# Kernel optimization log

Hardware: AMD Instinct MI355X
Metric: run time of the kernel (lower is better)

## Reference

```python
import jax, jax.numpy as jnp
import numpy as np

N_NODES = 50000
N_EDGES = 600000
D_IN = 128
H = 128
D_OUT = 1


def setup_inputs() -> dict:
    key = jax.random.key(0)
    ks = jax.random.split(key, 6)
    x = jax.random.normal(ks[0], (N_NODES, D_IN), dtype=jnp.float32)
    edge_index = jax.random.randint(ks[1], (2, N_EDGES), 0, N_NODES, dtype=jnp.int32)
    # Glorot-ish init for GCN weights
    W1 = jax.random.normal(ks[2], (D_IN, H), dtype=jnp.float32) / np.sqrt(D_IN)
    W2 = jax.random.normal(ks[3], (H, H), dtype=jnp.float32) / np.sqrt(H)
    W3 = jax.random.normal(ks[4], (H, D_OUT), dtype=jnp.float32) / np.sqrt(H)
    b1 = jnp.zeros((H,), jnp.float32)
    b2 = jnp.zeros((H,), jnp.float32)
    b3 = jnp.zeros((D_OUT,), jnp.float32)
    return {"x": x, "edge_index": edge_index, "W1": W1, "b1": b1,
            "W2": W2, "b2": b2, "W3": W3, "b3": b3}


def _gcn_layer(h, src, dst, norm, self_norm, W, b, n_nodes):
    # GCNConv: h' = D^{-1/2}(A+I)D^{-1/2} (h W) + b
    hw = h @ W                                        # [N, F_out]
    msg = hw[src] * norm[:, None]                     # [E, F_out] edge gather
    agg = jax.ops.segment_sum(msg, dst, num_segments=n_nodes)
    agg = agg + hw * self_norm[:, None]               # self-loop contribution
    return agg + b


def reference(x, edge_index, W1, b1, W2, b2, W3, b3):
    # NOTE: F.dropout treated as identity (deterministic eval reference).
    n = x.shape[0]
    src, dst = edge_index[0], edge_index[1]
    # symmetric normalization with self-loops (PyG gcn_norm, edge_weight=1)
    deg = jnp.zeros((n,), x.dtype).at[dst].add(1.0) + 1.0
    dis = jax.lax.rsqrt(deg)                          # deg^{-1/2}
    norm = dis[src] * dis[dst]                        # per-edge norm
    self_norm = dis * dis
    h = jax.nn.relu(_gcn_layer(x, src, dst, norm, self_norm, W1, b1, n))
    h = jax.nn.relu(_gcn_layer(h, src, dst, norm, self_norm, W2, b2, n))
    h = jax.nn.relu(_gcn_layer(h, src, dst, norm, self_norm, W3, b3, n))
    return h
```

## Files before the change

kernel.cpp:

```cpp
#include <hip/hip_runtime.h>
#include <hip/hip_fp16.h>


typedef _Float16 v8h __attribute__((ext_vector_type(8)));
typedef float v4f __attribute__((ext_vector_type(4)));

__global__ __launch_bounds__(256) void k_zero_wcast(int* __restrict__ cnt8, int n8,
                                                    int BZ,
                                                    const float* __restrict__ W1,
                                                    const float* __restrict__ W2,
                                                    __half* __restrict__ Wt1,
                                                    __half* __restrict__ Wt2) {
    int b = blockIdx.x;
    if (b < BZ) {
        int i = b * 256 + threadIdx.x;
        if (i < n8) cnt8[i] = 0;
    } else {
        int i = (b - BZ) * 256 + threadIdx.x;
        int k = i >> 7, c = i & 127;
        Wt1[c * 128 + k] = __float2half(W1[i]);
        Wt2[c * 128 + k] = __float2half(W2[i]);
    }
}

__global__ __launch_bounds__(256) void k_count_gemm(const int* __restrict__ dst,
                                                    int* __restrict__ cnt8,
                                                    int* __restrict__ rank, int nE,
                                                    int BE, int nN,
                                                    const float* __restrict__ X32,
                                                    const __half* __restrict__ Wt,
                                                    __half* __restrict__ HWS,
                                                    int nrows) {
    __shared__ __half xs[64 * 136];
    if (blockIdx.x < BE) {
        int e = blockIdx.x * 256 + threadIdx.x;
        if (e < nE) {
            int bank = blockIdx.x & 7;
            rank[e] = atomicAdd(&cnt8[bank * nN + dst[e]], 1);
        }
        return;
    }

    const int t = threadIdx.x;
    const int row0 = (blockIdx.x - BE) * 64;

#pragma unroll
    for (int i = 0; i < 8; ++i) {
        int f = t + i * 256;
        int r = f >> 5, k4 = f & 31;
        int gr = row0 + r;
        float4 v = make_float4(0.f, 0.f, 0.f, 0.f);
        if (gr < nrows) v = ((const float4*)X32)[(size_t)gr * 32 + k4];
        __half2 h01 = __float22half2_rn(make_float2(v.x, v.y));
        __half2 h23 = __float22half2_rn(make_float2(v.z, v.w));
        float2 packed;
        *(__half2*)&packed.x = h01;
        *(__half2*)&packed.y = h23;
        *(float2*)&xs[r * 136 + k4 * 4] = packed;
    }
    __syncthreads();

    const int w = t >> 6;
    const int l = t & 63;
    const int mrow = l & 15;
    const int kq = l >> 4;

    v8h a[4];
#pragma unroll
    for (int kk = 0; kk < 4; ++kk)
        a[kk] = *(const v8h*)&xs[(w * 16 + mrow) * 136 + kk * 32 + kq * 8];

    v4f acc[8];
#pragma unroll
    for (int c = 0; c < 8; ++c) acc[c] = (v4f){0.f, 0.f, 0.f, 0.f};

#pragma unroll
    for (int kk = 0; kk < 4; ++kk) {
#pragma unroll
        for (int c = 0; c < 8; ++c) {
            v8h b = *(const v8h*)&Wt[(size_t)(c * 16 + mrow) * 128 + kk * 32 + kq * 8];
            acc[c] = __builtin_amdgcn_mfma_f32_16x16x32_f16(a[kk], b, acc[c], 0, 0, 0);
        }
    }

#pragma unroll
    for (int c = 0; c < 8; ++c) {
#pragma unroll
        for (int r = 0; r < 4; ++r) {
            int grow = row0 + w * 16 + kq * 4 + r;
            if (grow < nrows)
                HWS[(size_t)grow * 128 + c * 16 + mrow] = __float2half(acc[c][r]);
        }
    }
}

__global__ __launch_bounds__(256) void k_scan_blk(const int* __restrict__ cnt8,
                                                  float* __restrict__ dis,
                                                  int* __restrict__ excl,
                                                  int* __restrict__ blk_sum, int nN) {
    __shared__ int sm[256];
    const int t = threadIdx.x;
    int i = blockIdx.x * 256 + t;
    int v = 0;
    if (i < nN) {
#pragma unroll
        for (int b = 0; b < 8; ++b) v += cnt8[b * nN + i];
        dis[i] = rsqrtf((float)v + 1.0f);
    }
    sm[t] = v;
    __syncthreads();
#pragma unroll
    for (int off = 1; off < 256; off <<= 1) {
        int x = (t >= off) ? sm[t - off] : 0;
        __syncthreads();
        sm[t] += x;
        __syncthreads();
    }
    if (i < nN) excl[i] = sm[t] - v;
    if (t == 255) blk_sum[blockIdx.x] = sm[255];
}

__global__ __launch_bounds__(256) void k_scan_add(const int* __restrict__ excl,
                                                  const int* __restrict__ blk_sum,
                                                  const int* __restrict__ cnt8,
                                                  int* __restrict__ row_ptr,
                                                  int* __restrict__ base8,
                                                  int nN, int nB) {
    __shared__ int sm[256];
    const int t = threadIdx.x;
    int v = (t < nB) ? blk_sum[t] : 0;
    sm[t] = v;
    __syncthreads();
#pragma unroll
    for (int off = 1; off < 256; off <<= 1) {
        int x = (t >= off) ? sm[t - off] : 0;
        __syncthreads();
        sm[t] += x;
        __syncthreads();
    }
    int i = blockIdx.x * 256 + t;
    if (i < nN) {
        int b = i >> 8;
        int rp = excl[i] + sm[b] - blk_sum[b];
        row_ptr[i] = rp;
        int off = rp;
#pragma unroll
        for (int bk = 0; bk < 8; ++bk) {
            base8[i * 8 + bk] = off;
            off += cnt8[bk * nN + i];
        }
    }
    if (i == 0) row_ptr[nN] = sm[255];
}

__global__ __launch_bounds__(256) void k_bin(const int* __restrict__ src,
                                             const int* __restrict__ dst,
                                             const int* __restrict__ rank,
                                             const int* __restrict__ base8,
                                             int* __restrict__ src_csr, int nE) {
    int e = blockIdx.x * 256 + threadIdx.x;
    if (e < nE) {
        int d = dst[e];
        int bank = blockIdx.x & 7;
        src_csr[base8[d * 8 + bank] + rank[e]] = src[e];
    }
}

__device__ __forceinline__ void add8(float acc[8], float4 r) {
    __half2* hp = (__half2*)&r;
#pragma unroll
    for (int k = 0; k < 4; ++k) {
        float2 f = __half22float2(hp[k]);
        acc[2 * k] += f.x;
        acc[2 * k + 1] += f.y;
    }
}

__device__ __forceinline__ void add8w(float acc[8], float4 r, float w) {
    __half2* hp = (__half2*)&r;
#pragma unroll
    for (int k = 0; k < 4; ++k) {
        float2 f = __half22float2(hp[k]);
        acc[2 * k] = fmaf(f.x, w, acc[2 * k]);
        acc[2 * k + 1] = fmaf(f.y, w, acc[2 * k + 1]);
    }
}

__device__ __forceinline__ void gather_row16(const float4* __restrict__ Hv,
                                             const int* __restrict__ row_ptr,
                                             const int* __restrict__ src_csr,
                                             int g, int f8, float acc[8]) {
    int beg = row_ptr[g], end = row_ptr[g + 1];
#pragma unroll
    for (int k = 0; k < 8; ++k) acc[k] = 0.f;
    add8(acc, Hv[(size_t)g * 16 + f8]);
    int e = beg;
    for (; e + 4 <= end; e += 4) {
        int s[4];
#pragma unroll
        for (int j = 0; j < 4; ++j) s[j] = src_csr[e + j];
        float4 r[4];
#pragma unroll
        for (int j = 0; j < 4; ++j) r[j] = Hv[(size_t)s[j] * 16 + f8];
#pragma unroll
        for (int j = 0; j < 4; ++j) add8(acc, r[j]);
    }
    for (; e < end; ++e) add8(acc, Hv[(size_t)src_csr[e] * 16 + f8]);
}

__device__ __forceinline__ void gather_row16w(const float4* __restrict__ Hv,
                                              const int* __restrict__ row_ptr,
                                              const int* __restrict__ src_csr,
                                              const float* __restrict__ dis,
                                              int g, float dg, int f8,
                                              float acc[8]) {
    int beg = row_ptr[g], end = row_ptr[g + 1];
#pragma unroll
    for (int k = 0; k < 8; ++k) acc[k] = 0.f;
    add8w(acc, Hv[(size_t)g * 16 + f8], dg);
    int e = beg;
    for (; e + 4 <= end; e += 4) {
        int s[4];
#pragma unroll
        for (int j = 0; j < 4; ++j) s[j] = src_csr[e + j];
        float wv[4];
#pragma unroll
        for (int j = 0; j < 4; ++j) wv[j] = dis[s[j]];
        float4 r[4];
#pragma unroll
        for (int j = 0; j < 4; ++j) r[j] = Hv[(size_t)s[j] * 16 + f8];
#pragma unroll
        for (int j = 0; j < 4; ++j) add8w(acc, r[j], wv[j]);
    }
    for (; e < end; ++e) {
        int s = src_csr[e];
        add8w(acc, Hv[(size_t)s * 16 + f8], dis[s]);
    }
}

__global__ __launch_bounds__(512) void k_gather_gemm(const __half* __restrict__ HWS1,
                                                     const int* __restrict__ row_ptr,
                                                     const int* __restrict__ src_csr,
                                                     const float* __restrict__ dis,
                                                     const float* __restrict__ bias,
                                                     const __half* __restrict__ Wt,
                                                     __half* __restrict__ HWS2,
                                                     int nN) {
    __shared__ __half xs[64 * 136];
    __shared__ int q;
    const int t = threadIdx.x;
    const int row0 = blockIdx.x * 64;
    const int l = t & 63;
    const int f8 = t & 15;
    const int qbase = l & 48;
    const float4* Hv = (const float4*)HWS1;

    float bv[8];
    *(float4*)&bv[0] = ((const float4*)bias)[f8 * 2];
    *(float4*)&bv[4] = ((const float4*)bias)[f8 * 2 + 1];

    if (t == 0) q = 0;
    __syncthreads();

    for (;;) {
        int lr = 0;
        if (f8 == 0) lr = atomicAdd(&q, 1);
        lr = __shfl(lr, qbase, 64);
        if (lr >= 64) break;
        int g = row0 + lr;
        float acc[8];
        __half2 h[4];
        if (g < nN) {
            float dn = dis[g];
            gather_row16w(Hv, row_ptr, src_csr, dis, g, dn, f8, acc);
#pragma unroll
            for (int k = 0; k < 4; ++k)
                h[k] = __float22half2_rn(make_float2(
                    fmaxf(acc[2 * k] * dn + bv[2 * k], 0.f),
                    fmaxf(acc[2 * k + 1] * dn + bv[2 * k + 1], 0.f)));
        } else {
#pragma unroll
            for (int k = 0; k < 4; ++k) h[k] = __float2half2_rn(0.f);
        }
        *(float4*)&xs[lr * 136 + f8 * 8] = *(float4*)h;
    }
    __syncthreads();

    const int w = t >> 6;
    const int mrow = l & 15;
    const int kq = l >> 4;
    const int rgrp = (w & 3) * 16;
    const int cgrp = (w >> 2) * 4;

    v8h a[4];
#pragma unroll
    for (int kk = 0; kk < 4; ++kk)
        a[kk] = *(const v8h*)&xs[(rgrp + mrow) * 136 + kk * 32 + kq * 8];

    v4f acc[4];
#pragma unroll
    for (int c = 0; c < 4; ++c) acc[c] = (v4f){0.f, 0.f, 0.f, 0.f};

#pragma unroll
    for (int kk = 0; kk < 4; ++kk) {
#pragma unroll
        for (int c = 0; c < 4; ++c) {
            v8h b = *(const v8h*)&Wt[(size_t)((cgrp + c) * 16 + mrow) * 128 + kk * 32 + kq * 8];
            acc[c] = __builtin_amdgcn_mfma_f32_16x16x32_f16(a[kk], b, acc[c], 0, 0, 0);
        }
    }

    float dn4[4];
#pragma unroll
    for (int r = 0; r < 4; ++r) {
        int grow = row0 + rgrp + kq * 4 + r;
        dn4[r] = (grow < nN) ? dis[grow] : 0.f;
    }
#pragma unroll
    for (int c = 0; c < 4; ++c) {
#pragma unroll
        for (int r = 0; r < 4; ++r) {
            int grow = row0 + rgrp + kq * 4 + r;
            if (grow < nN)
                HWS2[(size_t)grow * 128 + (cgrp + c) * 16 + mrow] =
                    __float2half(acc[c][r] * dn4[r]);
        }
    }
}

__global__ __launch_bounds__(256) void k_gather_gemv(const __half* __restrict__ HWS2,
                                                     const int* __restrict__ row_ptr,
                                                     const int* __restrict__ src_csr,
                                                     const float* __restrict__ dis,
                                                     const float* __restrict__ bias,
                                                     const float* __restrict__ W3,
                                                     float* __restrict__ hw3s, int nN) {
    int g = blockIdx.x * 16 + (threadIdx.x >> 4);
    if (g >= nN) return;
    int f8 = threadIdx.x & 15;
    float acc[8];
    gather_row16((const float4*)HWS2, row_ptr, src_csr, g, f8, acc);
    float dn = dis[g];
    float bv[8], w3[8];
    *(float4*)&bv[0] = ((const float4*)bias)[f8 * 2];
    *(float4*)&bv[4] = ((const float4*)bias)[f8 * 2 + 1];
    *(float4*)&w3[0] = ((const float4*)W3)[f8 * 2];
    *(float4*)&w3[4] = ((const float4*)W3)[f8 * 2 + 1];
    float sum = 0.f;
#pragma unroll
    for (int k = 0; k < 8; ++k)
        sum += fmaxf(acc[k] * dn + bv[k], 0.f) * w3[k];
#pragma unroll
    for (int off = 8; off > 0; off >>= 1) sum += __shfl_down(sum, off, 16);
    if (f8 == 0) hw3s[g] = sum * dn;
}

__global__ __launch_bounds__(256) void k_gather3(const float* __restrict__ hw3s,
                                                 const int* __restrict__ row_ptr,
                                                 const int* __restrict__ src_csr,
                                                 const float* __restrict__ dis,
                                                 const float* __restrict__ b3,
                                                 float* __restrict__ out, int nN) {
    int i = blockIdx.x * 256 + threadIdx.x;
    if (i >= nN) return;
    float acc = hw3s[i];
    int beg = row_ptr[i], end = row_ptr[i + 1];
    for (int e = beg; e < end; ++e) acc += hw3s[src_csr[e]];
    out[i] = fmaxf(acc * dis[i] + b3[0], 0.f);
}

extern "C" void kernel_launch(void* const* d_in, const int* in_sizes, int n_in,
                              void* d_out, int out_size, void* d_ws, size_t ws_size,
                              hipStream_t stream) {
    const float* x  = (const float*)d_in[0];
    const int*   ei = (const int*)d_in[1];
    const float* W1 = (const float*)d_in[2];
    const float* b1 = (const float*)d_in[3];
    const float* W2 = (const float*)d_in[4];
    const float* b2 = (const float*)d_in[5];
    const float* W3 = (const float*)d_in[6];
    const float* b3 = (const float*)d_in[7];

    const int nN = in_sizes[0] / 128;
    const int nE = in_sizes[1] / 2;
    const int* src = ei;
    const int* dst = ei + nE;

    const int nB = (nN + 255) / 256;

    char* p = (char*)d_ws;
    int*    cnt8     = (int*)p;           p += (size_t)nN * 8 * 4;
    int*    base8    = (int*)p;           p += (size_t)nN * 8 * 4;
    int*    excl     = (int*)p;           p += (size_t)nN * 4;
    int*    blk_sum  = (int*)p;           p += (size_t)(nB + 1) * 4;
    int*    row_ptr  = (int*)p;           p += (size_t)(nN + 1) * 4;
    int*    rank     = (int*)p;           p += (size_t)nE * 4;
    int*    src_csr  = (int*)p;           p += (size_t)nE * 4;
    float*  dis      = (float*)p;         p += (size_t)nN * 4;
    float*  hw3s     = (float*)p;         p += (size_t)nN * 4;
    p = (char*)(((uintptr_t)p + 255) & ~(uintptr_t)255);
    __half* Wt1      = (__half*)p;        p += (size_t)128 * 128 * 2;
    __half* Wt2      = (__half*)p;        p += (size_t)128 * 128 * 2;
    __half* bufA     = (__half*)p;        p += (size_t)nN * 128 * 2;
    p = (char*)(((uintptr_t)p + 255) & ~(uintptr_t)255);
    __half* bufB     = (__half*)p;        p += (size_t)nN * 128 * 2;

    const int BE  = (nE + 255) / 256;
    const int BN  = (nN + 255) / 256;
    const int BG  = (nN + 63) / 64;
    const int BGV = (nN + 15) / 16;
    const int BZ8 = (nN * 8 + 255) / 256;

    k_zero_wcast<<<BZ8 + 64, 256, 0, stream>>>(cnt8, nN * 8, BZ8, W1, W2, Wt1, Wt2);

    k_count_gemm<<<BE + BG, 256, 0, stream>>>(dst, cnt8, rank, nE, BE, nN,
                                              x, Wt1, bufA, nN);

    k_scan_blk<<<nB, 256, 0, stream>>>(cnt8, dis, excl, blk_sum, nN);
    k_scan_add<<<nB, 256, 0, stream>>>(excl, blk_sum, cnt8, row_ptr, base8, nN, nB);

    k_bin<<<BE, 256, 0, stream>>>(src, dst, rank, base8, src_csr, nE);

    k_gather_gemm<<<BG, 512, 0, stream>>>(bufA, row_ptr, src_csr, dis, b1, Wt2,
                                          bufB, nN);

    k_gather_gemv<<<BGV, 256, 0, stream>>>(bufB, row_ptr, src_csr, dis, b2, W3,
                                           hw3s, nN);

    k_gather3<<<BN, 256, 0, stream>>>(hw3s, row_ptr, src_csr, dis, b3,
                                      (float*)d_out, nN);
}
```

Baseline: 222.6 us.

## Prescale layer-1 GEMM output by dis and fuse it with CSR binning

```diff
diff --git a/kernel.cpp b/kernel.cpp
--- a/kernel.cpp
+++ b/kernel.cpp
@@ -23,26 +23,100 @@
     }
 }
 
-__global__ __launch_bounds__(256) void k_count_gemm(const int* __restrict__ dst,
-                                                    int* __restrict__ cnt8,
-                                                    int* __restrict__ rank, int nE,
-                                                    int BE, int nN,
-                                                    const float* __restrict__ X32,
-                                                    const __half* __restrict__ Wt,
-                                                    __half* __restrict__ HWS,
-                                                    int nrows) {
+__global__ __launch_bounds__(256) void k_count(const int* __restrict__ dst,
+                                               int* __restrict__ cnt8,
+                                               int* __restrict__ rank,
+                                               int nE, int nN) {
+    int e = blockIdx.x * 256 + threadIdx.x;
+    if (e < nE) {
+        int bank = blockIdx.x & 7;
+        rank[e] = atomicAdd(&cnt8[bank * nN + dst[e]], 1);
+    }
+}
+
+__global__ __launch_bounds__(256) void k_scan_blk(const int* __restrict__ cnt8,
+                                                  float* __restrict__ dis,
+                                                  int* __restrict__ excl,
+                                                  int* __restrict__ blk_sum, int nN) {
+    __shared__ int sm[256];
+    const int t = threadIdx.x;
+    int i = blockIdx.x * 256 + t;
+    int v = 0;
+    if (i < nN) {
+#pragma unroll
+        for (int b = 0; b < 8; ++b) v += cnt8[b * nN + i];
+        dis[i] = rsqrtf((float)v + 1.0f);
+    }
+    sm[t] = v;
+    __syncthreads();
+#pragma unroll
+    for (int off = 1; off < 256; off <<= 1) {
+        int x = (t >= off) ? sm[t - off] : 0;
+        __syncthreads();
+        sm[t] += x;
+        __syncthreads();
+    }
+    if (i < nN) excl[i] = sm[t] - v;
+    if (t == 255) blk_sum[blockIdx.x] = sm[255];
+}
+
+__global__ __launch_bounds__(256) void k_scan_add(const int* __restrict__ excl,
+                                                  const int* __restrict__ blk_sum,
+                                                  const int* __restrict__ cnt8,
+                                                  int* __restrict__ row_ptr,
+                                                  int* __restrict__ base8,
+                                                  int nN, int nB) {
+    __shared__ int sm[256];
+    const int t = threadIdx.x;
+    int v = (t < nB) ? blk_sum[t] : 0;
+    sm[t] = v;
+    __syncthreads();
+#pragma unroll
+    for (int off = 1; off < 256; off <<= 1) {
+        int x = (t >= off) ? sm[t - off] : 0;
+        __syncthreads();
+        sm[t] += x;
+        __syncthreads();
+    }
+    int i = blockIdx.x * 256 + t;
+    if (i < nN) {
+        int b = i >> 8;
+        int rp = excl[i] + sm[b] - blk_sum[b];
+        row_ptr[i] = rp;
+        int off = rp;
+#pragma unroll
+        for (int bk = 0; bk < 8; ++bk) {
+            base8[i * 8 + bk] = off;
+            off += cnt8[bk * nN + i];
+        }
+    }
+    if (i == 0) row_ptr[nN] = sm[255];
+}
+
+__global__ __launch_bounds__(256) void k_gemm_bin(const float* __restrict__ X32,
+                                                  const __half* __restrict__ Wt,
+                                                  const float* __restrict__ dis,
+                                                  __half* __restrict__ HWS,
+                                                  int nrows, int BG,
+                                                  const int* __restrict__ src,
+                                                  const int* __restrict__ dst,
+                                                  const int* __restrict__ rank,
+                                                  const int* __restrict__ base8,
+                                                  int* __restrict__ src_csr, int nE) {
     __shared__ __half xs[64 * 136];
-    if (blockIdx.x < BE) {
-        int e = blockIdx.x * 256 + threadIdx.x;
+    if (blockIdx.x >= BG) {
+        int eb = blockIdx.x - BG;
+        int e = eb * 256 + threadIdx.x;
         if (e < nE) {
-            int bank = blockIdx.x & 7;
-            rank[e] = atomicAdd(&cnt8[bank * nN + dst[e]], 1);
+            int d = dst[e];
+            int bank = eb & 7;
+            src_csr[base8[d * 8 + bank] + rank[e]] = src[e];
         }
         return;
     }
 
     const int t = threadIdx.x;
-    const int row0 = (blockIdx.x - BE) * 64;
+    const int row0 = blockIdx.x * 64;
 
 #pragma unroll
     for (int i = 0; i < 8; ++i) {
@@ -83,86 +157,21 @@
         }
     }
 
+    float dn[4];
+#pragma unroll
+    for (int r = 0; r < 4; ++r) {
+        int grow = row0 + w * 16 + kq * 4 + r;
+        dn[r] = (grow < nrows) ? dis[grow] : 0.f;
+    }
 #pragma unroll
     for (int c = 0; c < 8; ++c) {
 #pragma unroll
         for (int r = 0; r < 4; ++r) {
             int grow = row0 + w * 16 + kq * 4 + r;
             if (grow < nrows)
-                HWS[(size_t)grow * 128 + c * 16 + mrow] = __float2half(acc[c][r]);
-        }
-    }
-}
-
-__global__ __launch_bounds__(256) void k_scan_blk(const int* __restrict__ cnt8,
-                                                  float* __restrict__ dis,
-                                                  int* __restrict__ excl,
-                                                  int* __restrict__ blk_sum, int nN) {
-    __shared__ int sm[256];
-    const int t = threadIdx.x;
-    int i = blockIdx.x * 256 + t;
-    int v = 0;
-    if (i < nN) {
-#pragma unroll
-        for (int b = 0; b < 8; ++b) v += cnt8[b * nN + i];
-        dis[i] = rsqrtf((float)v + 1.0f);
-    }
-    sm[t] = v;
-    __syncthreads();
-#pragma unroll
-    for (int off = 1; off < 256; off <<= 1) {
-        int x = (t >= off) ? sm[t - off] : 0;
-        __syncthreads();
-        sm[t] += x;
-        __syncthreads();
-    }
-    if (i < nN) excl[i] = sm[t] - v;
-    if (t == 255) blk_sum[blockIdx.x] = sm[255];
-}
-
-__global__ __launch_bounds__(256) void k_scan_add(const int* __restrict__ excl,
-                                                  const int* __restrict__ blk_sum,
-                                                  const int* __restrict__ cnt8,
-                                                  int* __restrict__ row_ptr,
-                                                  int* __restrict__ base8,
-                                                  int nN, int nB) {
-    __shared__ int sm[256];
-    const int t = threadIdx.x;
-    int v = (t < nB) ? blk_sum[t] : 0;
-    sm[t] = v;
-    __syncthreads();
-#pragma unroll
-    for (int off = 1; off < 256; off <<= 1) {
-        int x = (t >= off) ? sm[t - off] : 0;
-        __syncthreads();
-        sm[t] += x;
-        __syncthreads();
-    }
-    int i = blockIdx.x * 256 + t;
-    if (i < nN) {
-        int b = i >> 8;
-        int rp = excl[i] + sm[b] - blk_sum[b];
-        row_ptr[i] = rp;
-        int off = rp;
-#pragma unroll
-        for (int bk = 0; bk < 8; ++bk) {
-            base8[i * 8 + bk] = off;
-            off += cnt8[bk * nN + i];
-        }
-    }
-    if (i == 0) row_ptr[nN] = sm[255];
-}
-
-__global__ __launch_bounds__(256) void k_bin(const int* __restrict__ src,
-                                             const int* __restrict__ dst,
-                                             const int* __restrict__ rank,
-                                             const int* __restrict__ base8,
-                                             int* __restrict__ src_csr, int nE) {
-    int e = blockIdx.x * 256 + threadIdx.x;
-    if (e < nE) {
-        int d = dst[e];
-        int bank = blockIdx.x & 7;
-        src_csr[base8[d * 8 + bank] + rank[e]] = src[e];
+                HWS[(size_t)grow * 128 + c * 16 + mrow] =
+                    __float2half(acc[c][r] * dn[r]);
+        }
     }
 }
 
@@ -173,16 +182,6 @@
         float2 f = __half22float2(hp[k]);
         acc[2 * k] += f.x;
         acc[2 * k + 1] += f.y;
-    }
-}
-
-__device__ __forceinline__ void add8w(float acc[8], float4 r, float w) {
-    __half2* hp = (__half2*)&r;
-#pragma unroll
-    for (int k = 0; k < 4; ++k) {
-        float2 f = __half22float2(hp[k]);
-        acc[2 * k] = fmaf(f.x, w, acc[2 * k]);
-        acc[2 * k + 1] = fmaf(f.y, w, acc[2 * k + 1]);
     }
 }
 
@@ -195,46 +194,28 @@
     for (int k = 0; k < 8; ++k) acc[k] = 0.f;
     add8(acc, Hv[(size_t)g * 16 + f8]);
     int e = beg;
-    for (; e + 4 <= end; e += 4) {
-        int s[4];
-#pragma unroll
-        for (int j = 0; j < 4; ++j) s[j] = src_csr[e + j];
-        float4 r[4];
-#pragma unroll
-        for (int j = 0; j < 4; ++j) r[j] = Hv[(size_t)s[j] * 16 + f8];
-#pragma unroll
-        for (int j = 0; j < 4; ++j) add8(acc, r[j]);
-    }
-    for (; e < end; ++e) add8(acc, Hv[(size_t)src_csr[e] * 16 + f8]);
-}
-
-__device__ __forceinline__ void gather_row16w(const float4* __restrict__ Hv,
-                                              const int* __restrict__ row_ptr,
-                                              const int* __restrict__ src_csr,
-                                              const float* __restrict__ dis,
-                                              int g, float dg, int f8,
-                                              float acc[8]) {
-    int beg = row_ptr[g], end = row_ptr[g + 1];
-#pragma unroll
-    for (int k = 0; k < 8; ++k) acc[k] = 0.f;
-    add8w(acc, Hv[(size_t)g * 16 + f8], dg);
-    int e = beg;
-    for (; e + 4 <= end; e += 4) {
-        int s[4];
-#pragma unroll
-        for (int j = 0; j < 4; ++j) s[j] = src_csr[e + j];
-        float wv[4];
-#pragma unroll
-        for (int j = 0; j < 4; ++j) wv[j] = dis[s[j]];
-        float4 r[4];
-#pragma unroll
-        for (int j = 0; j < 4; ++j) r[j] = Hv[(size_t)s[j] * 16 + f8];
-#pragma unroll
-        for (int j = 0; j < 4; ++j) add8w(acc, r[j], wv[j]);
-    }
-    for (; e < end; ++e) {
-        int s = src_csr[e];
-        add8w(acc, Hv[(size_t)s * 16 + f8], dis[s]);
+    for (; e + 8 <= end; e += 8) {
+        int s[8];
+#pragma unroll
+        for (int j = 0; j < 8; ++j) s[j] = src_csr[e + j];
+        float4 r[8];
+#pragma unroll
+        for (int j = 0; j < 8; ++j) r[j] = Hv[(size_t)s[j] * 16 + f8];
+#pragma unroll
+        for (int j = 0; j < 8; ++j) add8(acc, r[j]);
+    }
+    int rem = end - e;
+    if (rem > 0) {
+        int last = end - 1;
+        int s[8];
+#pragma unroll
+        for (int j = 0; j < 8; ++j) s[j] = src_csr[(e + j <= last) ? e + j : last];
+        float4 r[8];
+#pragma unroll
+        for (int j = 0; j < 8; ++j) r[j] = Hv[(size_t)s[j] * 16 + f8];
+#pragma unroll
+        for (int j = 0; j < 8; ++j)
+            if (j < rem) add8(acc, r[j]);
     }
 }
 
@@ -271,8 +252,8 @@
         float acc[8];
         __half2 h[4];
         if (g < nN) {
+            gather_row16(Hv, row_ptr, src_csr, g, f8, acc);
             float dn = dis[g];
-            gather_row16w(Hv, row_ptr, src_csr, dis, g, dn, f8, acc);
 #pragma unroll
             for (int k = 0; k < 4; ++k)
                 h[k] = __float22half2_rn(make_float2(
@@ -413,13 +394,13 @@
 
     k_zero_wcast<<<BZ8 + 64, 256, 0, stream>>>(cnt8, nN * 8, BZ8, W1, W2, Wt1, Wt2);
 
-    k_count_gemm<<<BE + BG, 256, 0, stream>>>(dst, cnt8, rank, nE, BE, nN,
-                                              x, Wt1, bufA, nN);
+    k_count<<<BE, 256, 0, stream>>>(dst, cnt8, rank, nE, nN);
 
     k_scan_blk<<<nB, 256, 0, stream>>>(cnt8, dis, excl, blk_sum, nN);
     k_scan_add<<<nB, 256, 0, stream>>>(excl, blk_sum, cnt8, row_ptr, base8, nN, nB);
 
-    k_bin<<<BE, 256, 0, stream>>>(src, dst, rank, base8, src_csr, nE);
+    k_gemm_bin<<<BG + BE, 256, 0, stream>>>(x, Wt1, dis, bufA, nN, BG,
+                                            src, dst, rank, base8, src_csr, nE);
 
     k_gather_gemm<<<BG, 512, 0, stream>>>(bufA, row_ptr, src_csr, dis, b1, Wt2,
                                           bufB, nN);
```

Result: faster. 217.6 us (-2.2%).
